# Kernel optimization log

Hardware: AMD Instinct MI355X
Metric: run time of the kernel (lower is better)

The kernel has to match this reference:

```python
import jax, jax.numpy as jnp
import numpy as np

N = 100000  # nodes (in_features)
D = 32      # out_features
E = 1600000 # edges


def setup_inputs() -> dict:
    key = jax.random.key(0)
    k1, k2, k3, k4, k5 = jax.random.split(key, 5)
    edge_row = jax.random.randint(k1, (E,), 0, N, dtype=jnp.int64)
    edge_col = jax.random.randint(k2, (E,), 0, N, dtype=jnp.int64)
    edge_val = jax.random.uniform(k3, (E,), dtype=jnp.float32)
    weight = jax.random.normal(k4, (N, D), dtype=jnp.float32)
    bias = jax.random.normal(k5, (D,), dtype=jnp.float32)
    return {"edge_row": edge_row, "edge_col": edge_col,
            "edge_val": edge_val, "weight": weight, "bias": bias}


def reference(edge_row, edge_col, edge_val, weight, bias):
    # out = adj @ weight + bias, adj given in COO form.
    # Gather weight rows per edge column, scale by edge value,
    # segment-sum into destination rows. [E, D] intermediate.
    contrib = edge_val[:, None] * jnp.take(weight, edge_col, axis=0)
    out = jax.ops.segment_sum(contrib, edge_row, num_segments=N)
    return out + bias
```

## Files before the change

kernel.cpp:

```cpp
#include <hip/hip_runtime.h>


#define FEAT 32
#define LOG_RPB 7
#define RPB (1 << LOG_RPB)
#define COLBITS 17
#define CMASK ((1u << COLBITS) - 1)
#define BMAX 1024
#define PCHUNK 4096
#define PTHREADS 1024
#define EPT (PCHUNK / PTHREADS)
#define CAPB 2560
#define CAP_MAX 32


__global__ __launch_bounds__(256) void gnn_zero(
    int* __restrict__ cursor, int* __restrict__ scnt, int B) {
    int i = blockIdx.x * 256 + threadIdx.x;
    if (i < B) cursor[i] = 0;
    if (i == B) *scnt = 0;
}

__global__ __launch_bounds__(PTHREADS) void gnn_part(
    const int* __restrict__ edge_row,
    const int* __restrict__ edge_col,
    const float* __restrict__ edge_val,
    int* __restrict__ cursor,
    float2* __restrict__ parts,
    float4* __restrict__ spill,
    int* __restrict__ scnt,
    int num_edges, int B) {
    __shared__ float2 lrec[PCHUNK];
    __shared__ unsigned short lbkt[PCHUNK];
    __shared__ int hcur[BMAX];
    __shared__ int st[BMAX];
    int t = threadIdx.x;
    hcur[t] = 0;
    __syncthreads();

    int e0 = blockIdx.x * PCHUNK;
    int cnt_chunk = num_edges - e0;
    if (cnt_chunk > PCHUNK) cnt_chunk = PCHUNK;

    int  r[EPT], c[EPT], bb[EPT], slot[EPT];
    float vv[EPT];
    int ebase = e0 + 4 * t;
    if (ebase + 3 < num_edges) {
        int4  r4 = *(const int4*)(edge_row + ebase);
        int4  c4 = *(const int4*)(edge_col + ebase);
        float4 v4 = *(const float4*)(edge_val + ebase);
        r[0] = r4.x; r[1] = r4.y; r[2] = r4.z; r[3] = r4.w;
        c[0] = c4.x; c[1] = c4.y; c[2] = c4.z; c[3] = c4.w;
        vv[0] = v4.x; vv[1] = v4.y; vv[2] = v4.z; vv[3] = v4.w;
    } else {
        #pragma unroll
        for (int k = 0; k < EPT; ++k) {
            int e = ebase + k;
            bool ok = e < num_edges;
            r[k]  = ok ? edge_row[e] : -1;
            c[k]  = ok ? edge_col[e] : 0;
            vv[k] = ok ? edge_val[e] : 0.f;
        }
    }
    #pragma unroll
    for (int k = 0; k < EPT; ++k) {
        if (r[k] >= 0) {
            bb[k] = r[k] >> LOG_RPB;
            slot[k] = atomicAdd(&hcur[bb[k]], 1);
        }
    }
    __syncthreads();

    int v = hcur[t];
    st[t] = v;
    __syncthreads();
    #pragma unroll
    for (int off = 1; off < BMAX; off <<= 1) {
        int u = (t >= off) ? st[t - off] : 0;
        __syncthreads();
        st[t] += u;
        __syncthreads();
    }
    int ex = st[t] - v;
    st[t] = ex;
    int rbase = 0;
    if (t < B && v) rbase = atomicAdd(&cursor[t], v);
    hcur[t] = rbase;
    __syncthreads();

    #pragma unroll
    for (int k = 0; k < EPT; ++k) {
        if (r[k] >= 0) {
            int pos = st[bb[k]] + slot[k];
            unsigned pk = (unsigned)c[k] |
                          ((unsigned)(r[k] & (RPB - 1)) << COLBITS);
            lrec[pos] = make_float2(__uint_as_float(pk), vv[k]);
            lbkt[pos] = (unsigned short)bb[k];
        }
    }
    __syncthreads();

    for (int i = t; i < cnt_chunk; i += PTHREADS) {
        int b2 = lbkt[i];
        float2 rec = lrec[i];
        int s = hcur[b2] + (i - st[b2]);
        if (s < CAPB) {
            parts[(long long)b2 * CAPB + s] = rec;
        } else {
            int si = atomicAdd(scnt, 1);
            unsigned pk = __float_as_uint(rec.x);
            spill[si] = make_float4(
                __uint_as_float((unsigned)(b2 << LOG_RPB) + (pk >> COLBITS)),
                __uint_as_float(pk & CMASK), rec.y, 0.f);
        }
    }
}

__global__ __launch_bounds__(512) void gnn_accum(
    const float2* __restrict__ parts,
    const int* __restrict__ cursor,
    const int* __restrict__ scnt,
    const float4* __restrict__ spill,
    const float* __restrict__ weight,
    const float* __restrict__ bias,
    float* __restrict__ out,
    int n_nodes) {
    __shared__ float2 srec[CAPB];
    __shared__ int h[RPB];
    __shared__ int rs[RPB + 1];
    int b = blockIdx.x, t = threadIdx.x;
    int n = cursor[b];
    int nspill = *scnt;
    int m = n < CAPB ? n : CAPB;
    const float2* p = parts + (long long)b * CAPB;

    float2 rec[CAPB / 512];
    int rl[CAPB / 512], slot[CAPB / 512];
    if (t < RPB) h[t] = 0;
    __syncthreads();
    #pragma unroll
    for (int k = 0; k < CAPB / 512; ++k) {
        int idx = t + k * 512;
        bool ok = idx < m;
        rec[k] = ok ? p[idx] : make_float2(0.f, 0.f);
        if (ok) {
            rl[k] = (int)((__float_as_uint(rec[k].x) >> COLBITS) & (RPB - 1));
            slot[k] = atomicAdd(&h[rl[k]], 1);
        }
    }
    __syncthreads();

    if (t < 64) {
        int a  = h[2 * t];
        int c2 = h[2 * t + 1];
        int pr = a + c2;
        int x = pr;
        #pragma unroll
        for (int off = 1; off < 64; off <<= 1) {
            int y = __shfl_up(x, off);
            if (t >= off) x += y;
        }
        int exc = x - pr;
        rs[2 * t] = exc;
        rs[2 * t + 1] = exc + a;
        if (t == 63) rs[RPB] = x;
    }
    __syncthreads();

    #pragma unroll
    for (int k = 0; k < CAPB / 512; ++k) {
        int idx = t + k * 512;
        if (idx < m) srec[rs[rl[k]] + slot[k]] = rec[k];
    }
    __syncthreads();

    int g = t >> 5;
    int f = t & 31;
    int row0 = b << LOG_RPB;
    float bf = bias[f];
    #pragma unroll 1
    for (int rr = 0; rr < 8; ++rr) {
        int rlc = (g << 3) + rr;
        int s = rs[rlc], e = rs[rlc + 1];
        float acc = 0.f;
        for (int j = s; j < e; j += 8) {
            float2 rc[8];
            float w[8];
            #pragma unroll
            for (int k = 0; k < 8; ++k) {
                int jj = j + k;
                rc[k] = srec[jj < e ? jj : s];
            }
            #pragma unroll
            for (int k = 0; k < 8; ++k)
                w[k] = weight[(__float_as_uint(rc[k].x) & CMASK) * FEAT + f];
            #pragma unroll
            for (int k = 0; k < 8; ++k)
                acc += (j + k < e) ? rc[k].y * w[k] : 0.f;
        }
        if (nspill > 0) {
            for (int i = 0; i < nspill; ++i) {
                float4 sp = spill[i];
                if ((int)__float_as_uint(sp.x) == row0 + rlc)
                    acc += sp.z *
                           weight[__float_as_uint(sp.y) * FEAT + f];
            }
        }
        int rrow = row0 + rlc;
        if (rrow < n_nodes)
            out[(long long)rrow * FEAT + f] = acc + bf;
    }
}


__global__ __launch_bounds__(256) void gnn_init(
    const float* __restrict__ bias, float* __restrict__ out,
    int* __restrict__ cnt, int total4, int n_nodes) {
    int i = blockIdx.x * blockDim.x + threadIdx.x;
    if (i < total4) {
        float4 bb = ((const float4*)bias)[i & 7];
        ((float4*)out)[i] = bb;
    }
    if (i < n_nodes) cnt[i] = 0;
}

__global__ __launch_bounds__(256) void gnn_bin(
    const int* __restrict__ edge_row,
    const int* __restrict__ edge_col,
    const float* __restrict__ edge_val,
    const float* __restrict__ weight,
    float2* __restrict__ bins,
    int* __restrict__ cnt,
    float* __restrict__ out,
    int num_edges, int cap) {
    int e = blockIdx.x * blockDim.x + threadIdx.x;
    if (e >= num_edges) return;
    int r = edge_row[e];
    int c = edge_col[e];
    float v = edge_val[e];
    int slot = atomicAdd(&cnt[r], 1);
    if (slot < cap) {
        bins[(long long)r * cap + slot] = make_float2(__int_as_float(c), v);
    } else {
        const float* w = weight + (long long)c * FEAT;
        #pragma unroll
        for (int f = 0; f < FEAT; ++f)
            atomicAdd(out + (long long)r * FEAT + f, v * w[f]);
    }
}

__global__ __launch_bounds__(256) void gnn_gather(
    const float2* __restrict__ bins,
    const int* __restrict__ cnt,
    const float* __restrict__ weight,
    float* __restrict__ out,
    int n_nodes, int cap) {
    int g = (blockIdx.x * blockDim.x + threadIdx.x) >> 5;
    int f = threadIdx.x & (FEAT - 1);
    if (g >= n_nodes) return;
    int n = cnt[g];
    n = n < cap ? n : cap;
    const float2* b = bins + (long long)g * cap;
    float a0 = 0.f, a1 = 0.f, a2 = 0.f, a3 = 0.f;
    int j = 0;
    for (; j + 4 <= n; j += 4) {
        float2 e0 = b[j], e1 = b[j + 1], e2 = b[j + 2], e3 = b[j + 3];
        a0 += e0.y * weight[(long long)__float_as_int(e0.x) * FEAT + f];
        a1 += e1.y * weight[(long long)__float_as_int(e1.x) * FEAT + f];
        a2 += e2.y * weight[(long long)__float_as_int(e2.x) * FEAT + f];
        a3 += e3.y * weight[(long long)__float_as_int(e3.x) * FEAT + f];
    }
    for (; j < n; ++j) {
        float2 e0 = b[j];
        a0 += e0.y * weight[(long long)__float_as_int(e0.x) * FEAT + f];
    }
    out[(long long)g * FEAT + f] += (a0 + a1) + (a2 + a3);
}


__global__ __launch_bounds__(256) void gnn_init_out(
    const float* __restrict__ bias, float* __restrict__ out, int total) {
    int i = blockIdx.x * blockDim.x + threadIdx.x;
    if (i < total) out[i] = bias[i & (FEAT - 1)];
}

__global__ __launch_bounds__(256) void gnn_scatter(
    const int* __restrict__ edge_row,
    const int* __restrict__ edge_col,
    const float* __restrict__ edge_val,
    const float* __restrict__ weight,
    float* __restrict__ out,
    int num_edges) {
    long long t = (long long)blockIdx.x * blockDim.x + threadIdx.x;
    int e = (int)(t >> 5);
    int f = (int)(t & (FEAT - 1));
    if (e < num_edges) {
        int r = edge_row[e];
        int c = edge_col[e];
        atomicAdd(out + r * FEAT + f, edge_val[e] * weight[c * FEAT + f]);
    }
}

extern "C" void kernel_launch(void* const* d_in, const int* in_sizes, int n_in,
                              void* d_out, int out_size, void* d_ws, size_t ws_size,
                              hipStream_t stream) {
    const int*   edge_row = (const int*)d_in[0];
    const int*   edge_col = (const int*)d_in[1];
    const float* edge_val = (const float*)d_in[2];
    const float* weight   = (const float*)d_in[3];
    const float* bias     = (const float*)d_in[4];
    float* out = (float*)d_out;

    const int E = in_sizes[0];
    const int total = out_size;
    const int N = total / FEAT;
    const int B = (N + RPB - 1) >> LOG_RPB;

    auto align256 = [](size_t x) { return (x + 255) & ~(size_t)255; };
    size_t cursor_off = 0;
    size_t scnt_off   = align256(cursor_off + (size_t)B * sizeof(int));
    size_t spill_off  = align256(scnt_off + sizeof(int));
    size_t parts_off  = align256(spill_off + (size_t)E * sizeof(float4));
    size_t need_v7    = parts_off + (size_t)B * CAPB * sizeof(float2);

    if (B >= 1 && B <= BMAX && N <= (1 << COLBITS) && E > 0 && ws_size >= need_v7) {
        int*    cursor = (int*)((char*)d_ws + cursor_off);
        int*    scnt   = (int*)((char*)d_ws + scnt_off);
        float4* spill  = (float4*)((char*)d_ws + spill_off);
        float2* parts  = (float2*)((char*)d_ws + parts_off);

        gnn_zero<<<(B + 1 + 255) / 256, 256, 0, stream>>>(cursor, scnt, B);
        gnn_part<<<(E + PCHUNK - 1) / PCHUNK, PTHREADS, 0, stream>>>(
            edge_row, edge_col, edge_val, cursor, parts, spill, scnt, E, B);
        gnn_accum<<<B, 512, 0, stream>>>(
            parts, cursor, scnt, spill, weight, bias, out, N);
        return;
    }

    size_t cnt_bytes = align256((size_t)N * sizeof(int));
    long long cap_ll = 0;
    if (ws_size > cnt_bytes)
        cap_ll = (long long)((ws_size - cnt_bytes) / ((size_t)N * sizeof(float2)));
    int cap = (int)(cap_ll > CAP_MAX ? CAP_MAX : cap_ll);

    if (cap >= 16) {
        int* cnt = (int*)d_ws;
        float2* bins = (float2*)((char*)d_ws + cnt_bytes);
        int total4 = total / 4;
        int init_threads = total4 > N ? total4 : N;
        gnn_init<<<(init_threads + 255) / 256, 256, 0, stream>>>(
            bias, out, cnt, total4, N);
        gnn_bin<<<(E + 255) / 256, 256, 0, stream>>>(
            edge_row, edge_col, edge_val, weight, bins, cnt, out, E, cap);
        long long gthreads = (long long)N * FEAT;
        gnn_gather<<<(int)((gthreads + 255) / 256), 256, 0, stream>>>(
            bins, cnt, weight, out, N, cap);
    } else {
        gnn_init_out<<<(total + 255) / 256, 256, 0, stream>>>(bias, out, total);
        long long threads = (long long)E * FEAT;
        gnn_scatter<<<(int)((threads + 255) / 256), 256, 0, stream>>>(
            edge_row, edge_col, edge_val, weight, out, E);
    }
}
```

Before: 125.5 us.

## Use wave-shuffle scan in partition and float4 weight gathers in accumulate

The partition kernel's 1024-wide block prefix sum, which used shared memory and a barrier per step, becomes a two-level scan: a wave-level shuffle scan followed by a scan over the 16 wave totals, which removes many barriers. The accumulate kernel now assigns 8 lanes per output row, each handling 4 features through float4 weight loads, accumulation and stores, instead of 32 lanes doing scalar loads. This cuts load instructions per gathered weight row and gives each thread more independent memory requests, at the cost of more registers per thread.

```diff
diff --git a/kernel.cpp b/kernel.cpp
--- a/kernel.cpp
+++ b/kernel.cpp
@@ -34,6 +34,7 @@
     __shared__ unsigned short lbkt[PCHUNK];
     __shared__ int hcur[BMAX];
     __shared__ int st[BMAX];
+    __shared__ int wtot[16], wbase[16];
     int t = threadIdx.x;
     hcur[t] = 0;
     __syncthreads();
@@ -72,16 +73,26 @@
     __syncthreads();
 
     int v = hcur[t];
-    st[t] = v;
-    __syncthreads();
-    #pragma unroll
-    for (int off = 1; off < BMAX; off <<= 1) {
-        int u = (t >= off) ? st[t - off] : 0;
-        __syncthreads();
-        st[t] += u;
-        __syncthreads();
-    }
-    int ex = st[t] - v;
+    int wid = t >> 6, lane = t & 63;
+    int x = v;
+    #pragma unroll
+    for (int off = 1; off < 64; off <<= 1) {
+        int y = __shfl_up(x, off);
+        if (lane >= off) x += y;
+    }
+    if (lane == 63) wtot[wid] = x;
+    __syncthreads();
+    if (t < 16) {
+        int w = wtot[t], xx = w;
+        #pragma unroll
+        for (int off = 1; off < 16; off <<= 1) {
+            int y = __shfl_up(xx, off);
+            if (t >= off) xx += y;
+        }
+        wbase[t] = xx - w;
+    }
+    __syncthreads();
+    int ex = x - v + wbase[wid];
     st[t] = ex;
     int rbase = 0;
     if (t < B && v) rbase = atomicAdd(&cursor[t], v);
@@ -174,41 +185,58 @@
     }
     __syncthreads();
 
-    int g = t >> 5;
-    int f = t & 31;
+    int g = t >> 3;
+    int l = t & 7;
     int row0 = b << LOG_RPB;
-    float bf = bias[f];
+    float4 bf4 = ((const float4*)bias)[l];
     #pragma unroll 1
-    for (int rr = 0; rr < 8; ++rr) {
-        int rlc = (g << 3) + rr;
+    for (int rr = 0; rr < 2; ++rr) {
+        int rlc = (g << 1) + rr;
         int s = rs[rlc], e = rs[rlc + 1];
-        float acc = 0.f;
+        float4 acc = make_float4(0.f, 0.f, 0.f, 0.f);
         for (int j = s; j < e; j += 8) {
-            float2 rc[8];
-            float w[8];
+            unsigned pk[8]; float vv[8];
             #pragma unroll
             for (int k = 0; k < 8; ++k) {
                 int jj = j + k;
-                rc[k] = srec[jj < e ? jj : s];
+                float2 rc = srec[jj < e ? jj : s];
+                pk[k] = __float_as_uint(rc.x);
+                vv[k] = rc.y;
             }
+            float4 w4[8];
             #pragma unroll
             for (int k = 0; k < 8; ++k)
-                w[k] = weight[(__float_as_uint(rc[k].x) & CMASK) * FEAT + f];
+                w4[k] = *(const float4*)(
+                    weight + (long long)(pk[k] & CMASK) * FEAT + (l << 2));
             #pragma unroll
-            for (int k = 0; k < 8; ++k)
-                acc += (j + k < e) ? rc[k].y * w[k] : 0.f;
+            for (int k = 0; k < 8; ++k) {
+                float sc = (j + k < e) ? vv[k] : 0.f;
+                acc.x += sc * w4[k].x;
+                acc.y += sc * w4[k].y;
+                acc.z += sc * w4[k].z;
+                acc.w += sc * w4[k].w;
+            }
         }
         if (nspill > 0) {
             for (int i = 0; i < nspill; ++i) {
                 float4 sp = spill[i];
-                if ((int)__float_as_uint(sp.x) == row0 + rlc)
-                    acc += sp.z *
-                           weight[__float_as_uint(sp.y) * FEAT + f];
+                if ((int)__float_as_uint(sp.x) == row0 + rlc) {
+                    float4 wz = *(const float4*)(
+                        weight + (long long)__float_as_uint(sp.y) * FEAT +
+                        (l << 2));
+                    acc.x += sp.z * wz.x;
+                    acc.y += sp.z * wz.y;
+                    acc.z += sp.z * wz.z;
+                    acc.w += sp.z * wz.w;
+                }
             }
         }
         int rrow = row0 + rlc;
-        if (rrow < n_nodes)
-            out[(long long)rrow * FEAT + f] = acc + bf;
+        if (rrow < n_nodes) {
+            float4 o = make_float4(acc.x + bf4.x, acc.y + bf4.y,
+                                   acc.z + bf4.z, acc.w + bf4.w);
+            *(float4*)(out + (long long)rrow * FEAT + (l << 2)) = o;
+        }
     }
 }
 
@@ -321,9 +349,9 @@
     size_t scnt_off   = align256(cursor_off + (size_t)B * sizeof(int));
     size_t spill_off  = align256(scnt_off + sizeof(int));
     size_t parts_off  = align256(spill_off + (size_t)E * sizeof(float4));
-    size_t need_v7    = parts_off + (size_t)B * CAPB * sizeof(float2);
-
-    if (B >= 1 && B <= BMAX && N <= (1 << COLBITS) && E > 0 && ws_size >= need_v7) {
+    size_t need_v8    = parts_off + (size_t)B * CAPB * sizeof(float2);
+
+    if (B >= 1 && B <= BMAX && N <= (1 << COLBITS) && E > 0 && ws_size >= need_v8) {
         int*    cursor = (int*)((char*)d_ws + cursor_off);
         int*    scnt   = (int*)((char*)d_ws + scnt_off);
         float4* spill  = (float4*)((char*)d_ws + spill_off);
```

New measurement: 122.1 us. -2.7%, faster.
